# Optimization experiments

Measured on AMD Instinct MI355X. Metric: run time of the kernel, lower is better.

Reference implementation:

```python
import jax, jax.numpy as jnp
import numpy as np
from jax import lax

SEQ_LENGTH = 32
B, I, O = 1024, 2048, 1024
DT = 1e-3
TAU_PRE, TAU_POST = 0.02, 0.02
ETA_PLUS, ETA_MINUS = 1e-3, 1e-3
W_MIN, W_MAX = -1.0, 1.0
TAU_MEM = 0.02
V_TH = 1.0


def setup_inputs() -> dict:
    key = jax.random.key(0)
    k1, k2, k3 = jax.random.split(key, 3)
    # Bernoulli(0.05) input spikes, rate-coded, reused each timestep
    input_spikes = (jax.random.uniform(k1, (B, I)) < 0.05).astype(jnp.float32)
    weight = jax.random.normal(k2, (O, I), dtype=jnp.float32) * (1.0 / np.sqrt(I))
    bias = jax.random.normal(k3, (O,), dtype=jnp.float32) * 0.01
    return {"input_spikes": input_spikes, "weight": weight, "bias": bias}


def reference(input_spikes, weight, bias):
    decay_pre = jnp.exp(jnp.float32(-DT / TAU_PRE))
    decay_post = jnp.exp(jnp.float32(-DT / TAU_POST))
    v_decay = jnp.exp(jnp.float32(-DT / TAU_MEM))

    b = input_spikes.shape[0]
    v0 = jnp.zeros((b, O), dtype=input_spikes.dtype)
    z0 = jnp.zeros((b, O), dtype=input_spikes.dtype)
    # STDPState(t_pre=1.0, t_post=1.0) broadcast to trace shapes
    tpre0 = jnp.ones((b, I), dtype=input_spikes.dtype)
    tpost0 = jnp.ones((b, O), dtype=input_spikes.dtype)

    def step(carry, _):
        v, w, tpre, tpost, _z = carry
        # linear projection with current (plastic) weights
        z_in = input_spikes @ w.T + bias  # [B, O]
        # LIF output neuron: decay, integrate, threshold, reset
        v = v * v_decay + z_in
        z_out = (v >= V_TH).astype(v.dtype)
        v = v * (1.0 - z_out)
        # STDP trace update: decay then accumulate spikes
        tpre = tpre * decay_pre + input_spikes
        tpost = tpost * decay_post + z_out
        # spike-gated eligibility outer products, summed over batch
        dw = (ETA_PLUS * jnp.einsum('bo,bi->oi', z_out, tpre)
              - ETA_MINUS * jnp.einsum('bo,bi->oi', tpost, input_spikes))
        w = jnp.clip(w + dw, W_MIN, W_MAX)
        return (v, w, tpre, tpost, z_out), None

    (v, w, tpre, tpost, z_out), _ = lax.scan(
        step, (v0, weight, tpre0, tpost0, z0), None, length=SEQ_LENGTH)
    return z_out, v, w
```

## Files before the change

### kernel.cpp

```cpp
#include <hip/hip_runtime.h>
#include <cmath>

#define SEQ 32
#define BB 1024
#define II 2048
#define OO 1024

typedef unsigned short ushortt;

__global__ void build_idx_rev(const float* __restrict__ x, ushortt* __restrict__ idxArr,
                              int* __restrict__ cntArr, int* __restrict__ rcnt,
                              ushortt* __restrict__ rev, ushortt* __restrict__ idxT) {
  int b = blockIdx.x;
  int lane = threadIdx.x;
  __shared__ ushortt sIdx[256];
  const float4* row4 = (const float4*)(x + (long)b * II);
  int base = 0;
  for (int c4 = 0; c4 < II / 256; ++c4) {
    float4 v = row4[c4 * 64 + lane];
    unsigned long long m0 = __ballot(v.x != 0.f);
    unsigned long long m1 = __ballot(v.y != 0.f);
    unsigned long long m2 = __ballot(v.z != 0.f);
    unsigned long long m3 = __ballot(v.w != 0.f);
    unsigned long long below = (1ull << lane) - 1ull;
    int pre = __popcll(m0 & below) + __popcll(m1 & below) +
              __popcll(m2 & below) + __popcll(m3 & below);
    int col0 = c4 * 256 + lane * 4;
    int pos = base + pre;
    if (v.x != 0.f) { if (pos < 256) { idxArr[(b << 8) + pos] = (ushortt)col0;       sIdx[pos] = (ushortt)col0; }       ++pos; }
    if (v.y != 0.f) { if (pos < 256) { idxArr[(b << 8) + pos] = (ushortt)(col0 + 1); sIdx[pos] = (ushortt)(col0 + 1); } ++pos; }
    if (v.z != 0.f) { if (pos < 256) { idxArr[(b << 8) + pos] = (ushortt)(col0 + 2); sIdx[pos] = (ushortt)(col0 + 2); } ++pos; }
    if (v.w != 0.f) { if (pos < 256) { idxArr[(b << 8) + pos] = (ushortt)(col0 + 3); sIdx[pos] = (ushortt)(col0 + 3); } ++pos; }
    base += __popcll(m0) + __popcll(m1) + __popcll(m2) + __popcll(m3);
  }
  int cnt = base < 256 ? base : 256;
  if (lane == 0) cntArr[b] = cnt;
  __syncthreads();
  {
    int j0 = lane * 4;
    ushort4 u;
    u.x = (j0 + 0 < cnt) ? sIdx[j0 + 0] : (ushortt)II;
    u.y = (j0 + 1 < cnt) ? sIdx[j0 + 1] : (ushortt)II;
    u.z = (j0 + 2 < cnt) ? sIdx[j0 + 2] : (ushortt)II;
    u.w = (j0 + 3 < cnt) ? sIdx[j0 + 3] : (ushortt)II;
    ((ushort4*)idxT)[(lane << 10) + b] = u;
  }
  for (int j = lane; j < cnt; j += 64) {
    int i = sIdx[j];
    int pos = atomicAdd(&rcnt[i], 1);
    if (pos < 128) rev[((long)i << 7) + pos] = (ushortt)b;
  }
}

__global__ void transpose2_f32(const float* __restrict__ zC, const float* __restrict__ vC,
                               float* __restrict__ oz, float* __restrict__ ov) {
  __shared__ float t[32][33];
  const float* src = blockIdx.z ? vC : zC;
  float* dst = blockIdx.z ? ov : oz;
  int c0 = blockIdx.x * 32, r0 = blockIdx.y * 32;
  int tx = threadIdx.x, ty = threadIdx.y;
#pragma unroll
  for (int k = 0; k < 4; k++)
    t[ty + k * 8][tx] = src[(long)(r0 + ty + k * 8) * BB + c0 + tx];
  __syncthreads();
#pragma unroll
  for (int k = 0; k < 4; k++)
    dst[(long)(c0 + ty + k * 8) * OO + r0 + tx] = t[tx][ty + k * 8];
}

__global__ __launch_bounds__(512, 8) void snn_kernel(
    const float* __restrict__ w, const float* __restrict__ bias,
    const ushortt* __restrict__ idxT, const int* __restrict__ cntArr,
    const int* __restrict__ rcnt, const ushortt* __restrict__ rev,
    const ushortt* __restrict__ idxArr,
    float* __restrict__ zC, float* __restrict__ vC, float* __restrict__ outw,
    float dec) {
  int o = blockIdx.x, tid = threadIdx.x, lane = tid & 63, wave = tid >> 6;
  __shared__ float2 wa[II + 1];
  __shared__ float mLb[II + 1];
  __shared__ int sList[BB];
  __shared__ float SnuD[BB];
  __shared__ int sCnt, sFlag, cFlag;
  float* mL = mLb;
  float* nT = mLb;
  float* Sfix = mLb;
  float* SAD = (float*)sList;

#pragma unroll
  for (int q = 0; q < 4; ++q) {
    int i = q * 512 + tid;
    wa[i] = make_float2(w[(long)o * II + i], 0.f);
    nT[i] = (float)rcnt[i];
  }
#pragma unroll
  for (int k = 0; k < 2; ++k) SnuD[k * 512 + tid] = 0.f;
  if (tid == 0) {
    sFlag = 0; cFlag = 0;
    wa[II] = make_float2(0.f, 0.f);
    nT[II] = 0.f;
  }

  int jmax[2];
#pragma unroll
  for (int k = 0; k < 2; ++k) {
    int c = cntArr[k * 512 + wave * 64 + lane];
#pragma unroll
    for (int off = 32; off > 0; off >>= 1) c = max(c, __shfl_xor(c, off));
    jmax[k] = c;
  }
  float bo = bias[o];
  unsigned clipped = 0;
  bool everSpk = false;
  float p = 1.f, u = 1.f;
  __syncthreads();

  const ushort4* tpb = (const ushort4*)idxT;
  double S[2];
  float Snu[2], SA[2], v4[2], zk[2];
#pragma unroll
  for (int k = 0; k < 2; ++k) {
    int b = k * 512 + tid;
    double s = 0.0;
    float sn = 0.f;
    int jm4 = (jmax[k] + 3) >> 2;
    const ushort4* tp = tpb + b;
    for (int g = 0; g < jm4; ++g) {
      ushort4 u0 = tp[(g << 10)];
      s += (double)wa[u0.x].x; sn += nT[u0.x];
      s += (double)wa[u0.y].x; sn += nT[u0.y];
      s += (double)wa[u0.z].x; sn += nT[u0.z];
      s += (double)wa[u0.w].x; sn += nT[u0.w];
    }
    S[k] = s; Snu[k] = sn;
    SA[k] = 0.f; v4[k] = 0.f; zk[k] = 0.f;
  }
  __syncthreads();
#pragma unroll
  for (int k = 0; k < 2; ++k) {
    int b = k * 512 + tid;
    Sfix[b] = 0.f; SAD[b] = 0.f;
  }

  for (int t = 0; t < SEQ; ++t) {
    p *= dec; u *= dec; u += 1.f;
    float spre = u - p;
    int local = 0;
#pragma unroll
    for (int k = 0; k < 2; ++k) {
      float zin = (float)S[k] + bo;
      float nv = v4[k] * dec + zin;
      float z = (nv >= 1.f) ? 1.f : 0.f;
      nv = nv * (1.f - z);
      v4[k] = nv; zk[k] = z;
      if (z != 0.f) local = 1;
    }
    if (local) sFlag = 1;
    __syncthreads();
    int spk = sFlag;

    if (!spk) {
#pragma unroll
      for (int q = 0; q < 4; ++q) {
        int i = q * 512 + tid;
        bool already = (clipped >> q) & 1u;
        float n = 0.f, atn = 0.f, fix = 0.f;
        bool cl = false;
        if (!already) {
          float2 tq = wa[i];
          n = (float)rcnt[i];
          atn = everSpk ? (dec * tq.y) : 0.f;
          float dw = -(1e-3f * (p * n + atn));
          float pre = tq.x + dw;
          float wv = fminf(fmaxf(pre, -1.f), 1.f);
          cl = (pre <= -1.f);
          if (cl) {
            clipped |= 1u << q;
            fix = (-1.f - tq.x) - dw;
            wa[i] = make_float2(wv, 0.f);
          } else {
            wa[i] = make_float2(wv, atn);
          }
        }
        unsigned long long m = __ballot(cl);
        if (m) {
          if (lane == 0) cFlag = 1;
          while (m) {
            int src = __builtin_ctzll(m);
            m &= m - 1;
            int ii = __shfl(i, src);
            float fx = __shfl(fix, src);
            float mn = -__shfl(n, src);
            float ma = -__shfl(atn, src);
            int rc = rcnt[ii];
            const ushortt* rp = rev + ((long)ii << 7);
            for (int r = lane; r < rc; r += 64) {
              int b2 = rp[r];
              atomicAdd(&Sfix[b2], fx);
              atomicAdd(&SnuD[b2], mn);
              if (everSpk) atomicAdd(&SAD[b2], ma);
            }
          }
        }
      }
      __syncthreads();
      float coefP = 1e-3f * p;
      if (cFlag) {
#pragma unroll
        for (int k = 0; k < 2; ++k) {
          int b = k * 512 + tid;
          S[k] = S[k] - (double)coefP * (double)Snu[k]
                      - (double)1e-3f * (double)(dec * SA[k])
                      + (double)Sfix[b];
          SA[k] = dec * SA[k] + SAD[b];
          Snu[k] = Snu[k] + SnuD[b];
          Sfix[b] = 0.f; SnuD[b] = 0.f; SAD[b] = 0.f;
        }
      } else {
#pragma unroll
        for (int k = 0; k < 2; ++k) {
          S[k] = S[k] - (double)coefP * (double)Snu[k]
                      - (double)1e-3f * (double)(dec * SA[k]);
          SA[k] = dec * SA[k];
        }
      }
      if (tid == 0) { sFlag = 0; cFlag = 0; }
      __syncthreads();
    } else {
      everSpk = true;
      if (tid == 0) sCnt = 0;
      __syncthreads();
#pragma unroll
      for (int k = 0; k < 2; ++k)
        if (zk[k] != 0.f) { int pos = atomicAdd(&sCnt, 1); sList[pos] = k * 512 + tid; }
#pragma unroll
      for (int q = 0; q < 4; ++q) mL[q * 512 + tid] = 0.f;
      __syncthreads();
      int ns = sCnt;
      for (int s = wave; s < ns; s += 8) {
        int b = sList[s];
        int cbb = cntArr[b];
        const ushortt* ip = idxArr + (b << 8);
        for (int j = lane; j < cbb; j += 64)
          atomicAdd(&mL[ip[j]], 1.f);
      }
      __syncthreads();
      float cv = (float)ns;
#pragma unroll
      for (int q = 0; q < 4; ++q) {
        int i = q * 512 + tid;
        float2 tq = wa[i];
        float mt = mL[i];
        float atn = dec * tq.y + mt;
        float n = (float)rcnt[i];
        float dw = 1e-3f * (p * cv + spre * mt) - 1e-3f * (p * n + atn);
        float pre = tq.x + dw;
        float wv = fminf(fmaxf(pre, -1.f), 1.f);
        bool cl = (pre <= -1.f);
        bool was = (clipped >> q) & 1u;
        if (cl) clipped |= 1u << q; else clipped &= ~(1u << q);
        wa[i] = make_float2(wv, cl ? 0.f : atn);
        bool flip = (cl != was);
        float dn = cl ? -n : n;
        unsigned long long m = __ballot(flip);
        while (m) {
          int src = __builtin_ctzll(m);
          m &= m - 1;
          int ii = __shfl(i, src);
          float d = __shfl(dn, src);
          int rc = rcnt[ii];
          const ushortt* rp = rev + ((long)ii << 7);
          for (int r = lane; r < rc; r += 64)
            atomicAdd(&SnuD[rp[r]], d);
        }
      }
      __syncthreads();
#pragma unroll
      for (int k = 0; k < 2; ++k) {
        int b = k * 512 + tid;
        double s = 0.0;
        float sa = 0.f;
        int jm4 = (jmax[k] + 3) >> 2;
        const ushort4* tp = tpb + b;
        for (int g = 0; g < jm4; ++g) {
          ushort4 u0 = tp[(g << 10)];
          float2 e0 = wa[u0.x], e1 = wa[u0.y], e2 = wa[u0.z], e3 = wa[u0.w];
          s += (double)e0.x; sa += e0.y;
          s += (double)e1.x; sa += e1.y;
          s += (double)e2.x; sa += e2.y;
          s += (double)e3.x; sa += e3.y;
        }
        S[k] = s; SA[k] = sa;
        Snu[k] = Snu[k] + SnuD[b];
        SnuD[b] = 0.f;
        Sfix[b] = 0.f; SAD[b] = 0.f;
      }
      if (tid == 0) { sFlag = 0; cFlag = 0; }
      __syncthreads();
    }
  }

  __syncthreads();
#pragma unroll
  for (int q = 0; q < 4; ++q) outw[(long)o * II + q * 512 + tid] = wa[q * 512 + tid].x;
#pragma unroll
  for (int k = 0; k < 2; ++k) {
    int b = k * 512 + tid;
    zC[(long)o * BB + b] = zk[k];
    vC[(long)o * BB + b] = v4[k];
  }
}

extern "C" void kernel_launch(void* const* d_in, const int* in_sizes, int n_in,
                              void* d_out, int out_size, void* d_ws, size_t ws_size,
                              hipStream_t stream) {
  const float* x = (const float*)d_in[0];
  const float* w = (const float*)d_in[1];
  const float* bias = (const float*)d_in[2];
  float* out = (float*)d_out;

  char* ws = (char*)d_ws;
  ushortt* idxArr = (ushortt*)(ws + 0);
  int* cntArr = (int*)(ws + 524288);
  ushortt* idxT = (ushortt*)(ws + 528384);
  int* rcnt = (int*)(ws + 1060864);
  ushortt* rev = (ushortt*)(ws + 1069056);
  float* zC = (float*)(ws + 1593344);
  float* vC = (float*)(ws + 5787648);

  hipMemsetAsync(rcnt, 0, II * sizeof(int), stream);
  build_idx_rev<<<BB, 64, 0, stream>>>(x, idxArr, cntArr, rcnt, rev, idxT);

  const float dec = (float)exp(-0.05);

  snn_kernel<<<OO, 512, 0, stream>>>(w, bias, idxT, cntArr, rcnt, rev, idxArr,
                                     zC, vC, out + 2 * BB * OO, dec);

  transpose2_f32<<<dim3(BB / 32, OO / 32, 2), dim3(32, 8), 0, stream>>>(zC, vC, out, out + BB * OO);
}
```

Baseline: 280.2 us.

## Replace full resum after spiking steps with incremental delta update of row sums

After a step where any output neuron spiked, the kernel no longer resums full weights and eligibility values in double precision over each batch row's active inputs. It encodes each input's spike-count increment and clip state into one shared float array and computes per-row deltas from it. Clip transitions and upper clips are pushed to affected rows through reverse-index atomics into new correction buffers. The packed float2 weight/eligibility array is split into separate arrays, which adds shared memory and float rounding drift in the incremental sums.

```diff
diff --git a/kernel.cpp b/kernel.cpp
--- a/kernel.cpp
+++ b/kernel.cpp
@@ -76,34 +76,42 @@
     float* __restrict__ zC, float* __restrict__ vC, float* __restrict__ outw,
     float dec) {
   int o = blockIdx.x, tid = threadIdx.x, lane = tid & 63, wave = tid >> 6;
-  __shared__ float2 wa[II + 1];
+  __shared__ float wL[II + 1];
+  __shared__ float aG[II];
   __shared__ float mLb[II + 1];
-  __shared__ int sList[BB];
+  __shared__ ushortt sList[BB];
   __shared__ float SnuD[BB];
+  __shared__ float SfxSp[BB];
+  __shared__ float SadSp[BB];
   __shared__ int sCnt, sFlag, cFlag;
+  float* nT = mLb;
   float* mL = mLb;
-  float* nT = mLb;
   float* Sfix = mLb;
-  float* SAD = (float*)sList;
+  float* SAD = SadSp;
 
 #pragma unroll
   for (int q = 0; q < 4; ++q) {
     int i = q * 512 + tid;
-    wa[i] = make_float2(w[(long)o * II + i], 0.f);
+    wL[i] = w[(long)o * II + i];
+    aG[i] = 0.f;
     nT[i] = (float)rcnt[i];
   }
 #pragma unroll
-  for (int k = 0; k < 2; ++k) SnuD[k * 512 + tid] = 0.f;
+  for (int k = 0; k < 2; ++k) {
+    int b = k * 512 + tid;
+    SnuD[b] = 0.f; SfxSp[b] = 0.f; SadSp[b] = 0.f;
+  }
   if (tid == 0) {
     sFlag = 0; cFlag = 0;
-    wa[II] = make_float2(0.f, 0.f);
-    nT[II] = 0.f;
+    wL[II] = 0.f; nT[II] = 0.f;
   }
 
   int jmax[2];
+  float cntf[2];
 #pragma unroll
   for (int k = 0; k < 2; ++k) {
-    int c = cntArr[k * 512 + wave * 64 + lane];
+    int c = cntArr[k * 512 + tid];
+    cntf[k] = (float)c;
 #pragma unroll
     for (int off = 32; off > 0; off >>= 1) c = max(c, __shfl_xor(c, off));
     jmax[k] = c;
@@ -116,7 +124,7 @@
 
   const ushort4* tpb = (const ushort4*)idxT;
   double S[2];
-  float Snu[2], SA[2], v4[2], zk[2];
+  float Snu[2], Nb[2], SA[2], v4[2], zk[2];
 #pragma unroll
   for (int k = 0; k < 2; ++k) {
     int b = k * 512 + tid;
@@ -126,20 +134,16 @@
     const ushort4* tp = tpb + b;
     for (int g = 0; g < jm4; ++g) {
       ushort4 u0 = tp[(g << 10)];
-      s += (double)wa[u0.x].x; sn += nT[u0.x];
-      s += (double)wa[u0.y].x; sn += nT[u0.y];
-      s += (double)wa[u0.z].x; sn += nT[u0.z];
-      s += (double)wa[u0.w].x; sn += nT[u0.w];
+      s += (double)wL[u0.x]; sn += nT[u0.x];
+      s += (double)wL[u0.y]; sn += nT[u0.y];
+      s += (double)wL[u0.z]; sn += nT[u0.z];
+      s += (double)wL[u0.w]; sn += nT[u0.w];
     }
-    S[k] = s; Snu[k] = sn;
+    S[k] = s; Snu[k] = sn; Nb[k] = sn;
     SA[k] = 0.f; v4[k] = 0.f; zk[k] = 0.f;
   }
   __syncthreads();
-#pragma unroll
-  for (int k = 0; k < 2; ++k) {
-    int b = k * 512 + tid;
-    Sfix[b] = 0.f; SAD[b] = 0.f;
-  }
+  Sfix[tid] = 0.f; Sfix[512 + tid] = 0.f;
 
   for (int t = 0; t < SEQ; ++t) {
     p *= dec; u *= dec; u += 1.f;
@@ -166,20 +170,21 @@
         float n = 0.f, atn = 0.f, fix = 0.f;
         bool cl = false;
         if (!already) {
-          float2 tq = wa[i];
           n = (float)rcnt[i];
-          atn = everSpk ? (dec * tq.y) : 0.f;
+          atn = everSpk ? (dec * aG[i]) : 0.f;
           float dw = -(1e-3f * (p * n + atn));
-          float pre = tq.x + dw;
+          float wold = wL[i];
+          float pre = wold + dw;
           float wv = fminf(fmaxf(pre, -1.f), 1.f);
           cl = (pre <= -1.f);
           if (cl) {
             clipped |= 1u << q;
-            fix = (-1.f - tq.x) - dw;
-            wa[i] = make_float2(wv, 0.f);
-          } else {
-            wa[i] = make_float2(wv, atn);
+            fix = (-1.f - wold) - dw;
+            if (everSpk) aG[i] = 0.f;
+          } else if (everSpk) {
+            aG[i] = atn;
           }
+          wL[i] = wv;
         }
         unsigned long long m = __ballot(cl);
         if (m) {
@@ -231,9 +236,10 @@
       __syncthreads();
 #pragma unroll
       for (int k = 0; k < 2; ++k)
-        if (zk[k] != 0.f) { int pos = atomicAdd(&sCnt, 1); sList[pos] = k * 512 + tid; }
+        if (zk[k] != 0.f) { int pos = atomicAdd(&sCnt, 1); sList[pos] = (ushortt)(k * 512 + tid); }
 #pragma unroll
       for (int q = 0; q < 4; ++q) mL[q * 512 + tid] = 0.f;
+      if (tid == 0) mLb[II] = 1.0f;
       __syncthreads();
       int ns = sCnt;
       for (int s = wave; s < ns; s += 8) {
@@ -248,52 +254,83 @@
 #pragma unroll
       for (int q = 0; q < 4; ++q) {
         int i = q * 512 + tid;
-        float2 tq = wa[i];
         float mt = mL[i];
-        float atn = dec * tq.y + mt;
+        float atn = dec * aG[i] + mt;
         float n = (float)rcnt[i];
         float dw = 1e-3f * (p * cv + spre * mt) - 1e-3f * (p * n + atn);
-        float pre = tq.x + dw;
+        float wold = wL[i];
+        float pre = wold + dw;
         float wv = fminf(fmaxf(pre, -1.f), 1.f);
         bool cl = (pre <= -1.f);
         bool was = (clipped >> q) & 1u;
         if (cl) clipped |= 1u << q; else clipped &= ~(1u << q);
-        wa[i] = make_float2(wv, cl ? 0.f : atn);
+        wL[i] = wv;
+        aG[i] = cl ? 0.f : atn;
+        mL[i] = was ? -(mt + 1.f) : (mt + 1.f);
+        bool hic = (pre >= 1.f);
         bool flip = (cl != was);
+        float dS = cl ? ((-1.f - wold) - dw) : dw;
         float dn = cl ? -n : n;
+        float dsa = cl ? -atn : mt;
         unsigned long long m = __ballot(flip);
         while (m) {
           int src = __builtin_ctzll(m);
           m &= m - 1;
           int ii = __shfl(i, src);
-          float d = __shfl(dn, src);
+          float a1 = __shfl(dS, src);
+          float a2 = __shfl(dn, src);
+          float a3 = __shfl(dsa, src);
+          int rc = rcnt[ii];
+          const ushortt* rp = rev + ((long)ii << 7);
+          for (int r = lane; r < rc; r += 64) {
+            int b2 = rp[r];
+            atomicAdd(&SfxSp[b2], a1);
+            atomicAdd(&SnuD[b2], a2);
+            atomicAdd(&SadSp[b2], a3);
+          }
+        }
+        unsigned long long mh = __ballot(hic);
+        while (mh) {
+          int src = __builtin_ctzll(mh);
+          mh &= mh - 1;
+          int ii = __shfl(i, src);
+          float a1 = 1.f - __shfl(pre, src);
           int rc = rcnt[ii];
           const ushortt* rp = rev + ((long)ii << 7);
           for (int r = lane; r < rc; r += 64)
-            atomicAdd(&SnuD[rp[r]], d);
+            atomicAdd(&SfxSp[rp[r]], a1);
         }
       }
       __syncthreads();
 #pragma unroll
       for (int k = 0; k < 2; ++k) {
         int b = k * 512 + tid;
-        double s = 0.0;
-        float sa = 0.f;
+        float G = 0.f, GC = 0.f, cC = 0.f;
         int jm4 = (jmax[k] + 3) >> 2;
         const ushort4* tp = tpb + b;
         for (int g = 0; g < jm4; ++g) {
           ushort4 u0 = tp[(g << 10)];
-          float2 e0 = wa[u0.x], e1 = wa[u0.y], e2 = wa[u0.z], e3 = wa[u0.w];
-          s += (double)e0.x; sa += e0.y;
-          s += (double)e1.x; sa += e1.y;
-          s += (double)e2.x; sa += e2.y;
-          s += (double)e3.x; sa += e3.y;
-        }
-        S[k] = s; SA[k] = sa;
+          float e0 = mL[u0.x], e1 = mL[u0.y], e2 = mL[u0.z], e3 = mL[u0.w];
+          float a0 = fabsf(e0) - 1.f, a1 = fabsf(e1) - 1.f;
+          float a2 = fabsf(e2) - 1.f, a3 = fabsf(e3) - 1.f;
+          G += a0 + a1 + a2 + a3;
+          if (e0 < 0.f) { GC += a0; cC += 1.f; }
+          if (e1 < 0.f) { GC += a1; cC += 1.f; }
+          if (e2 < 0.f) { GC += a2; cC += 1.f; }
+          if (e3 < 0.f) { GC += a3; cC += 1.f; }
+        }
+        float NC = Nb[k] - Snu[k];
+        float d_all = 1e-3f * (p * cv * cntf[k] + spre * G)
+                    - 1e-3f * (p * Nb[k] + dec * SA[k] + G);
+        float d_cor = -1e-3f * (p * cv * cC + spre * GC)
+                    + 1e-3f * (p * NC + GC);
+        S[k] = S[k] + (double)d_all + (double)d_cor + (double)SfxSp[b];
+        SA[k] = dec * SA[k] + (G - GC) + SadSp[b];
         Snu[k] = Snu[k] + SnuD[b];
-        SnuD[b] = 0.f;
-        Sfix[b] = 0.f; SAD[b] = 0.f;
-      }
+        SfxSp[b] = 0.f; SadSp[b] = 0.f; SnuD[b] = 0.f;
+      }
+      __syncthreads();
+      Sfix[tid] = 0.f; Sfix[512 + tid] = 0.f;
       if (tid == 0) { sFlag = 0; cFlag = 0; }
       __syncthreads();
     }
@@ -301,7 +338,7 @@
 
   __syncthreads();
 #pragma unroll
-  for (int q = 0; q < 4; ++q) outw[(long)o * II + q * 512 + tid] = wa[q * 512 + tid].x;
+  for (int q = 0; q < 4; ++q) outw[(long)o * II + q * 512 + tid] = wL[q * 512 + tid];
 #pragma unroll
   for (int k = 0; k < 2; ++k) {
     int b = k * 512 + tid;
```

Measured after the change: 306.8 us. 1.1x slower.
